# Performance work log

Measured on AMD Instinct MI355X. Metric: run time of the kernel, lower is better.

The kernel has to match this reference:

```python
import jax, jax.numpy as jnp
import numpy as np
import math

N_HEAD = 16
N_EMBD = 1024
N_LATENTS = 64
HEAD_DIM = N_EMBD // N_HEAD  # 64
ROPE_THETA = 10000.0


def setup_inputs() -> dict:
    key = jax.random.key(0)
    ks = jax.random.split(key, 6)
    B, T = 4, 4096
    x = jax.random.normal(ks[0], (B, T, N_EMBD), dtype=jnp.float32)
    # torch Linear weights applied as x @ W with W: [in, out] (equivalent up to init)
    s = 1.0 / math.sqrt(N_EMBD)
    Wk = jax.random.normal(ks[1], (N_EMBD, N_EMBD), dtype=jnp.float32) * s
    Wv = jax.random.normal(ks[2], (N_EMBD, N_EMBD), dtype=jnp.float32) * s
    Wg = jax.random.normal(ks[3], (N_EMBD, N_HEAD * N_LATENTS), dtype=jnp.float32) * s
    Wp = jax.random.normal(ks[4], (N_EMBD, N_EMBD), dtype=jnp.float32) * s
    latent_q = jax.random.normal(ks[5], (1, N_LATENTS, N_HEAD, HEAD_DIM), dtype=jnp.float32)
    return {"x": x, "latent_q": latent_q, "Wk": Wk, "Wv": Wv, "Wg": Wg, "Wp": Wp}


def _rope_interleaved(k, theta):
    # k: [B, T, H, D]; interleaved pairs rotated by position-dependent angles
    B, T, H, D = k.shape
    inv_freq = 1.0 / (theta ** (jnp.arange(0, D, 2, dtype=jnp.float32) / D))  # [D/2]
    ang = jnp.arange(T, dtype=jnp.float32)[:, None] * inv_freq[None, :]       # [T, D/2]
    cos = jnp.cos(ang)[None, :, None, :]
    sin = jnp.sin(ang)[None, :, None, :]
    k2 = k.reshape(B, T, H, D // 2, 2)
    kr = jnp.stack([k2[..., 0] * cos - k2[..., 1] * sin,
                    k2[..., 0] * sin + k2[..., 1] * cos], axis=-1)
    return kr.reshape(B, T, H, D).astype(k.dtype)


def reference(x, latent_q, Wk, Wv, Wg, Wp):
    B, T, C = x.shape
    H, D, L = N_HEAD, HEAD_DIM, N_LATENTS
    k = (x @ Wk).reshape(B, T, H, D)
    v = (x @ Wv).reshape(B, T, H, D)
    gates = jax.nn.softmax((x @ Wg).reshape(B, T, H, L), axis=-1)  # [B,T,H,L]
    k = _rope_interleaved(k, ROPE_THETA)
    q = jnp.broadcast_to(latent_q, (B, L, H, D)).transpose(0, 2, 1, 3)  # [B,H,L,D]
    kt = k.transpose(0, 2, 1, 3)  # [B,H,T,D]
    vt = v.transpose(0, 2, 1, 3)  # [B,H,T,D]
    scale = 1.0 / jnp.sqrt(jnp.asarray(D, dtype=x.dtype))
    scores = jnp.einsum('bhld,bhtd->bhlt', q, kt) * scale  # [B,H,L,T]
    # PyTorch SDPA is_causal with L_q != L_kv: top-left aligned tril(ones(L, T))
    causal = jnp.arange(T)[None, :] <= jnp.arange(L)[:, None]  # [L,T]
    scores = jnp.where(causal[None, None], scores, -jnp.inf)
    attn = jax.nn.softmax(scores, axis=-1)
    attn_out = jnp.einsum('bhlt,bhtd->bhld', attn, vt)  # [B,H,L,D]
    gates_t = gates.transpose(0, 2, 1, 3)  # [B,H,T,L]
    weighted = jnp.einsum('bhld,bhtl->bhtd', attn_out, gates_t)  # [B,H,T,D]
    out = weighted.transpose(0, 2, 1, 3).reshape(B, T, C)
    return out @ Wp
```

## Files before the change

### kernel.cpp

```cpp
#include <hip/hip_runtime.h>
#include <hip/hip_bf16.h>


typedef __attribute__((ext_vector_type(8))) short bf16x8;
typedef __attribute__((ext_vector_type(4))) float f32x4;
typedef __attribute__((ext_vector_type(4))) unsigned short us4;

__device__ __forceinline__ void gll16(const void* g, void* l) {
  __builtin_amdgcn_global_load_lds((const __attribute__((address_space(1))) void*)g,
                                   (__attribute__((address_space(3))) void*)l, 16, 0, 0);
}

__global__ __launch_bounds__(256)
void prep_kernel(const float* __restrict__ x, __hip_bfloat16* __restrict__ xb,
                 const float* __restrict__ Wg, const float* __restrict__ Wk,
                 const float* __restrict__ Wv, const float* __restrict__ Wp,
                 __hip_bfloat16* __restrict__ WgT, __hip_bfloat16* __restrict__ WkT,
                 __hip_bfloat16* __restrict__ WvT, __hip_bfloat16* __restrict__ WpT) {
  const int bid = blockIdx.x, tid = threadIdx.x;
  if (bid < 2048) {
    const int stride = 2048 * 256;
    for (int i = bid * 256 + tid; i < 4194304; i += stride) {
      float4 f = reinterpret_cast<const float4*>(x)[i];
      union { __hip_bfloat16 h[4]; us4 v; } u;
      u.h[0] = __float2bfloat16(f.x);
      u.h[1] = __float2bfloat16(f.y);
      u.h[2] = __float2bfloat16(f.z);
      u.h[3] = __float2bfloat16(f.w);
      reinterpret_cast<us4*>(xb)[i] = u.v;
    }
  } else {
    const int t = bid - 2048;
    const int z = t >> 10, rem = t & 1023;
    const float* W = (z == 0) ? Wg : ((z == 1) ? Wk : ((z == 2) ? Wv : Wp));
    __hip_bfloat16* Wt = (z == 0) ? WgT : ((z == 1) ? WkT : ((z == 2) ? WvT : WpT));
    __shared__ float tile[32][33];
    const int bx = (rem & 31) * 32, by = (rem >> 5) * 32;
    const int tx = tid & 31, ty = tid >> 5;
    #pragma unroll
    for (int j = 0; j < 32; j += 8)
      tile[ty + j][tx] = W[(size_t)(by + ty + j) * 1024 + bx + tx];
    __syncthreads();
    #pragma unroll
    for (int j = 0; j < 32; j += 8)
      Wt[(size_t)(bx + ty + j) * 1024 + by + tx] = __float2bfloat16(tile[tx][ty + j]);
  }
}

__global__ __launch_bounds__(256, 4)
void gemm128d(const __hip_bfloat16* __restrict__ A, const __hip_bfloat16* __restrict__ Bt,
              __hip_bfloat16* __restrict__ G) {
  __shared__ __align__(16) unsigned short SA[2][128 * 32];
  __shared__ __align__(16) unsigned short SB[2][128 * 32];
  const int tid = threadIdx.x;
  const int lane = tid & 63;
  const int w = tid >> 6;
  const int wm = w >> 1, wn = w & 1;
  const int lr = lane & 15, lk = lane >> 4;
  const int m0 = blockIdx.x * 128, n0 = blockIdx.y * 128;
  const int K = 1024;

  f32x4 acc[4][4] = {};

  auto STAGE = [&](int bsel, int kt) {
    #pragma unroll
    for (int r = 0; r < 2; ++r) {
      int c = r * 256 + tid;
      int row = c >> 2, slot = c & 3;
      int gs = slot ^ ((row >> 1) & 3);
      gll16(A + (size_t)(m0 + row) * K + kt + gs * 8, (char*)&SA[bsel][0] + c * 16);
      gll16(Bt + (size_t)(n0 + row) * K + kt + gs * 8, (char*)&SB[bsel][0] + c * 16);
    }
  };

  STAGE(0, 0);
  __syncthreads();

  int buf = 0;
  for (int t = 0; t < 32; ++t) {
    if (t + 1 < 32) STAGE(buf ^ 1, (t + 1) << 5);

    bf16x8 bfr[4];
    #pragma unroll
    for (int ni = 0; ni < 4; ++ni) {
      int row = wn * 64 + ni * 16 + lr;
      int ch = lk ^ ((row >> 1) & 3);
      bfr[ni] = *(const bf16x8*)&SB[buf][row * 32 + ch * 8];
    }
    #pragma unroll
    for (int mi = 0; mi < 4; ++mi) {
      int row = wm * 64 + mi * 16 + lr;
      int ch = lk ^ ((row >> 1) & 3);
      bf16x8 a = *(const bf16x8*)&SA[buf][row * 32 + ch * 8];
      #pragma unroll
      for (int ni = 0; ni < 4; ++ni)
        acc[mi][ni] = __builtin_amdgcn_mfma_f32_16x16x32_bf16(a, bfr[ni], acc[mi][ni], 0, 0, 0);
    }
    __syncthreads();
    buf ^= 1;
  }

  #pragma unroll
  for (int mi = 0; mi < 4; ++mi) {
    #pragma unroll
    for (int jj = 0; jj < 4; ++jj) {
      float mx = -3.0e38f;
      #pragma unroll
      for (int ni = 0; ni < 4; ++ni) mx = fmaxf(mx, acc[mi][ni][jj]);
      mx = fmaxf(mx, __shfl_xor(mx, 1));
      mx = fmaxf(mx, __shfl_xor(mx, 2));
      mx = fmaxf(mx, __shfl_xor(mx, 4));
      mx = fmaxf(mx, __shfl_xor(mx, 8));
      float e[4];
      float s = 0.f;
      #pragma unroll
      for (int ni = 0; ni < 4; ++ni) { e[ni] = __expf(acc[mi][ni][jj] - mx); s += e[ni]; }
      s += __shfl_xor(s, 1);
      s += __shfl_xor(s, 2);
      s += __shfl_xor(s, 4);
      s += __shfl_xor(s, 8);
      float inv = 1.0f / s;
      int r = m0 + wm * 64 + mi * 16 + lk * 4 + jj;
      #pragma unroll
      for (int ni = 0; ni < 4; ++ni)
        G[(size_t)r * 1024 + n0 + wn * 64 + ni * 16 + lr] = __float2bfloat16(e[ni] * inv);
    }
  }
}

__global__ __launch_bounds__(512, 2)
void gemm256o(const __hip_bfloat16* __restrict__ A, const __hip_bfloat16* __restrict__ Bt,
              float* __restrict__ Cv, int K, int ldc,
              long long astride, long long bstride, long long cstride) {
  __shared__ __align__(16) unsigned short SA[2][256 * 64];
  __shared__ __align__(16) unsigned short SB[2][256 * 64];
  const int tid = threadIdx.x;
  const int lane = tid & 63;
  const int w = tid >> 6;
  const int wm = w >> 2, wn = w & 3;
  const int lr = lane & 15, lk = lane >> 4;
  const int m0 = blockIdx.x * 256, n0 = blockIdx.y * 256;
  const long long b = blockIdx.z;
  const __hip_bfloat16* Ab = A + b * astride;
  const __hip_bfloat16* Bb = Bt + b * bstride;

  f32x4 acc[8][4] = {};

  const int NT = K >> 6;
  int buf = 0;

  auto STAGE = [&](int bsel, int kt) {
    #pragma unroll
    for (int r = 0; r < 4; ++r) {
      int c = r * 512 + tid;
      int row = c >> 3, slot = c & 7;
      int gch = slot ^ (row & 7);
      gll16(Ab + (size_t)(m0 + row) * K + kt + gch * 8, (char*)&SA[bsel][0] + c * 16);
      gll16(Bb + (size_t)(n0 + row) * K + kt + gch * 8, (char*)&SB[bsel][0] + c * 16);
    }
  };

  STAGE(0, 0);
  __syncthreads();

  for (int t = 0; t < NT; ++t) {
    if (t + 1 < NT) STAGE(buf ^ 1, (t + 1) << 6);

    bf16x8 bfr[2][4];
    #pragma unroll
    for (int kk = 0; kk < 2; ++kk)
      #pragma unroll
      for (int ni = 0; ni < 4; ++ni) {
        int row = wn * 64 + ni * 16 + lr;
        int ch = (kk * 4 + lk) ^ (row & 7);
        bfr[kk][ni] = *(const bf16x8*)&SB[buf][row * 64 + ch * 8];
      }
    #pragma unroll
    for (int mi = 0; mi < 8; ++mi) {
      int row = wm * 128 + mi * 16 + lr;
      int ch0 = lk ^ (row & 7);
      int ch1 = (4 + lk) ^ (row & 7);
      bf16x8 a0 = *(const bf16x8*)&SA[buf][row * 64 + ch0 * 8];
      bf16x8 a1 = *(const bf16x8*)&SA[buf][row * 64 + ch1 * 8];
      #pragma unroll
      for (int ni = 0; ni < 4; ++ni)
        acc[mi][ni] = __builtin_amdgcn_mfma_f32_16x16x32_bf16(a0, bfr[0][ni], acc[mi][ni], 0, 0, 0);
      #pragma unroll
      for (int ni = 0; ni < 4; ++ni)
        acc[mi][ni] = __builtin_amdgcn_mfma_f32_16x16x32_bf16(a1, bfr[1][ni], acc[mi][ni], 0, 0, 0);
    }
    __syncthreads();
    buf ^= 1;
  }

  float* C = Cv + b * cstride;
  #pragma unroll
  for (int mi = 0; mi < 8; ++mi) {
    int r = m0 + wm * 128 + mi * 16 + lk * 4;
    #pragma unroll
    for (int ni = 0; ni < 4; ++ni) {
      int c = n0 + wn * 64 + ni * 16 + lr;
      #pragma unroll
      for (int jj = 0; jj < 4; ++jj)
        C[(size_t)(r + jj) * ldc + c] = acc[mi][ni][jj];
    }
  }
}

__global__ __launch_bounds__(256)
void gemm_kv(const __hip_bfloat16* __restrict__ A, const __hip_bfloat16* __restrict__ Bt,
             float* __restrict__ kvp) {
  __shared__ __align__(16) unsigned short As[128 * 32];
  __shared__ __align__(16) unsigned short Bs[128 * 32];
  const int tid = threadIdx.x;
  const int lane = tid & 63;
  const int w = tid >> 6;
  const int wm = w >> 1, wn = w & 1;
  const int lr = lane & 15, lk = lane >> 4;
  const int m0 = blockIdx.x * 128, n0 = blockIdx.y * 128;
  const int ks = blockIdx.z;
  const int K = 1024;

  f32x4 acc[4][4] = {};
  const int r0 = tid >> 2;
  const int c8 = (tid & 3) * 8;

  auto xrow = [&](int rg) { return (size_t)(rg >> 6) * 4096 + (rg & 63); };

  for (int ki = 0; ki < 4; ++ki) {
    int kt = ks * 128 + ki * 32;
    __syncthreads();
    gll16(A + xrow(m0 + r0) * K + kt + c8,      (char*)As + (w * 64) * 16);
    gll16(Bt + (size_t)(n0 + r0) * K + kt + c8, (char*)Bs + (w * 64) * 16);
    gll16(A + xrow(m0 + 64 + r0) * K + kt + c8,      (char*)As + (256 + w * 64) * 16);
    gll16(Bt + (size_t)(n0 + 64 + r0) * K + kt + c8, (char*)Bs + (256 + w * 64) * 16);
    __syncthreads();

    bf16x8 af[4], bf[4];
    #pragma unroll
    for (int mi = 0; mi < 4; ++mi)
      af[mi] = *(const bf16x8*)&As[(wm * 64 + mi * 16 + lr) * 32 + lk * 8];
    #pragma unroll
    for (int ni = 0; ni < 4; ++ni)
      bf[ni] = *(const bf16x8*)&Bs[(wn * 64 + ni * 16 + lr) * 32 + lk * 8];
    #pragma unroll
    for (int mi = 0; mi < 4; ++mi)
      #pragma unroll
      for (int ni = 0; ni < 4; ++ni)
        acc[mi][ni] = __builtin_amdgcn_mfma_f32_16x16x32_bf16(af[mi], bf[ni], acc[mi][ni], 0, 0, 0);
  }

  float* C = kvp + (size_t)ks * 256 * 2048;
  #pragma unroll
  for (int mi = 0; mi < 4; ++mi) {
    int r = m0 + wm * 64 + mi * 16 + lk * 4;
    #pragma unroll
    for (int ni = 0; ni < 4; ++ni) {
      int c = n0 + wn * 64 + ni * 16 + lr;
      #pragma unroll
      for (int jj = 0; jj < 4; ++jj)
        C[(size_t)(r + jj) * 2048 + c] = acc[mi][ni][jj];
    }
  }
}

__global__ __launch_bounds__(256)
void attn_mt(const float* __restrict__ kvp, const float* __restrict__ lq,
             const __hip_bfloat16* __restrict__ WpT, __hip_bfloat16* __restrict__ Mt) {
  const int ct = blockIdx.x, h = blockIdx.y, b = blockIdx.z;
  __shared__ float Ks[64][64];
  __shared__ float Vs[64][64];
  __shared__ float S[64][65];
  __shared__ float Pt[64][65];
  __shared__ __align__(16) unsigned short SW[256 * 64];
  __shared__ __align__(16) unsigned short SAo[64 * 64];
  const int tid = threadIdx.x;
  const int lane = tid & 63;
  const int w = tid >> 6;
  const int lr = lane & 15, lk = lane >> 4;

  #pragma unroll
  for (int j = 0; j < 8; ++j) {
    int c2 = j * 256 + tid;
    int row = c2 >> 3, slot = c2 & 7;
    int gch = slot ^ (row & 7);
    gll16(WpT + (size_t)(ct * 256 + row) * 1024 + h * 64 + gch * 8, (char*)SW + c2 * 16);
  }

  {
    int r = tid >> 4;
    int c4 = (tid & 15) * 4;
    int i0 = c4 >> 1;
    float inv0 = exp2f(-13.287712379549449f * ((float)i0 * (1.0f / 32.0f)));
    float inv1 = exp2f(-13.287712379549449f * ((float)(i0 + 1) * (1.0f / 32.0f)));
    #pragma unroll
    for (int j = 0; j < 4; ++j) {
      int row = j * 16 + r;
      float4 kf = make_float4(0.f, 0.f, 0.f, 0.f);
      float4 vf = make_float4(0.f, 0.f, 0.f, 0.f);
      #pragma unroll
      for (int ks = 0; ks < 8; ++ks) {
        const float* base = kvp + ((size_t)ks * 256 + b * 64 + row) * 2048 + h * 64;
        float4 kp = *(const float4*)(base + c4);
        float4 vp = *(const float4*)(base + 1024 + c4);
        kf.x += kp.x; kf.y += kp.y; kf.z += kp.z; kf.w += kp.w;
        vf.x += vp.x; vf.y += vp.y; vf.z += vp.z; vf.w += vp.w;
      }
      float a0 = (float)row * inv0, a1 = (float)row * inv1;
      float s0 = sinf(a0), c0 = cosf(a0), s1 = sinf(a1), c1 = cosf(a1);
      *(float4*)&Ks[row][c4] = make_float4(kf.x * c0 - kf.y * s0, kf.x * s0 + kf.y * c0,
                                           kf.z * c1 - kf.w * s1, kf.z * s1 + kf.w * c1);
      *(float4*)&Vs[row][c4] = vf;
    }
  }
  __syncthreads();

  {
    const int l = tid & 63;
    float q[64];
    const float4* lq4 = (const float4*)(lq + ((size_t)l * 16 + h) * 64);
    #pragma unroll
    for (int i = 0; i < 16; ++i) {
      float4 f = lq4[i];
      q[4 * i] = f.x; q[4 * i + 1] = f.y; q[4 * i + 2] = f.z; q[4 * i + 3] = f.w;
    }
    #pragma unroll
    for (int tl = 0; tl < 16; ++tl) {
      int t = w * 16 + tl;
      float a = 0.f;
      #pragma unroll
      for (int d4 = 0; d4 < 16; ++d4) {
        float4 kf = *(const float4*)&Ks[t][d4 * 4];
        a += q[4 * d4] * kf.x + q[4 * d4 + 1] * kf.y + q[4 * d4 + 2] * kf.z + q[4 * d4 + 3] * kf.w;
      }
      S[l][t] = a * 0.125f;
    }
  }
  __syncthreads();

  {
    const int l = tid >> 2, c = tid & 3;
    float sv[16];
    float mx = -3.0e38f;
    #pragma unroll
    for (int i = 0; i < 16; ++i) {
      int t = c * 16 + i;
      sv[i] = S[l][t];
      if (t <= l) mx = fmaxf(mx, sv[i]);
    }
    mx = fmaxf(mx, __shfl_xor(mx, 1));
    mx = fmaxf(mx, __shfl_xor(mx, 2));
    float sum = 0.f;
    float e[16];
    #pragma unroll
    for (int i = 0; i < 16; ++i) {
      int t = c * 16 + i;
      e[i] = (t <= l) ? __expf(sv[i] - mx) : 0.f;
      sum += e[i];
    }
    sum += __shfl_xor(sum, 1);
    sum += __shfl_xor(sum, 2);
    float inv = 1.0f / sum;
    #pragma unroll
    for (int i = 0; i < 16; ++i) Pt[c * 16 + i][l] = e[i] * inv;
  }
  __syncthreads();

  {
    const int l = tid & 63;
    float o[16];
    #pragma unroll
    for (int i = 0; i < 16; ++i) o[i] = 0.f;
    for (int t = 0; t < 64; ++t) {
      float p = Pt[t][l];
      #pragma unroll
      for (int d4 = 0; d4 < 4; ++d4) {
        float4 vf = *(const float4*)&Vs[t][w * 16 + d4 * 4];
        o[4 * d4]     += p * vf.x;
        o[4 * d4 + 1] += p * vf.y;
        o[4 * d4 + 2] += p * vf.z;
        o[4 * d4 + 3] += p * vf.w;
      }
    }
    union { __hip_bfloat16 hh[8]; bf16x8 v; } p0, p1;
    #pragma unroll
    for (int i = 0; i < 8; ++i) { p0.hh[i] = __float2bfloat16(o[i]); p1.hh[i] = __float2bfloat16(o[8 + i]); }
    *(bf16x8*)&SAo[l * 64 + ((2 * w) ^ (l & 7)) * 8]     = p0.v;
    *(bf16x8*)&SAo[l * 64 + ((2 * w + 1) ^ (l & 7)) * 8] = p1.v;
  }
  __syncthreads();

  f32x4 acc[4][4] = {};
  bf16x8 bfr[2][4];
  #pragma unroll
  for (int kk = 0; kk < 2; ++kk)
    #pragma unroll
    for (int ni = 0; ni < 4; ++ni) {
      int row = ni * 16 + lr;
      int ch = (kk * 4 + lk) ^ (row & 7);
      bfr[kk][ni] = *(const bf16x8*)&SAo[row * 64 + ch * 8];
    }
  #pragma unroll
  for (int mi = 0; mi < 4; ++mi) {
    int row = w * 64 + mi * 16 + lr;
    int ch0 = lk ^ (row & 7);
    int ch1 = (4 + lk) ^ (row & 7);
    bf16x8 a0 = *(const bf16x8*)&SW[row * 64 + ch0 * 8];
    bf16x8 a1 = *(const bf16x8*)&SW[row * 64 + ch1 * 8];
    #pragma unroll
    for (int ni = 0; ni < 4; ++ni)
      acc[mi][ni] = __builtin_amdgcn_mfma_f32_16x16x32_bf16(a0, bfr[0][ni], acc[mi][ni], 0, 0, 0);
    #pragma unroll
    for (int ni = 0; ni < 4; ++ni)
      acc[mi][ni] = __builtin_amdgcn_mfma_f32_16x16x32_bf16(a1, bfr[1][ni], acc[mi][ni], 0, 0, 0);
  }

  #pragma unroll
  for (int mi = 0; mi < 4; ++mi) {
    int c = ct * 256 + w * 64 + mi * 16 + lk * 4;
    #pragma unroll
    for (int ni = 0; ni < 4; ++ni) {
      int l = ni * 16 + lr;
      #pragma unroll
      for (int jj = 0; jj < 4; ++jj)
        Mt[((size_t)b * 1024 + c + jj) * 1024 + h * 64 + l] = __float2bfloat16(acc[mi][ni][jj]);
    }
  }
}

extern "C" void kernel_launch(void* const* d_in, const int* in_sizes, int n_in,
                              void* d_out, int out_size, void* d_ws, size_t ws_size,
                              hipStream_t stream) {
  const float* x  = (const float*)d_in[0];
  const float* lq = (const float*)d_in[1];
  const float* Wk = (const float*)d_in[2];
  const float* Wv = (const float*)d_in[3];
  const float* Wg = (const float*)d_in[4];
  const float* Wp = (const float*)d_in[5];
  float* out = (float*)d_out;

  char* w = (char*)d_ws;
  __hip_bfloat16* xb   = (__hip_bfloat16*)(w);
  __hip_bfloat16* G    = (__hip_bfloat16*)(w + 33554432);
  __hip_bfloat16* WgT  = (__hip_bfloat16*)(w + 67108864);
  __hip_bfloat16* WkvT = (__hip_bfloat16*)(w + 69206016);
  __hip_bfloat16* WpT  = (__hip_bfloat16*)(w + 73400320);
  __hip_bfloat16* Mt   = (__hip_bfloat16*)(w + 75497472);
  float* kvp = out;

  prep_kernel<<<6144, 256, 0, stream>>>(x, xb, Wg, Wk, Wv, Wp,
                                        WgT, WkvT, WkvT + 1024 * 1024, WpT);

  gemm128d<<<dim3(128, 8), 256, 0, stream>>>(xb, WgT, G);

  gemm_kv<<<dim3(2, 16, 8), 256, 0, stream>>>(xb, WkvT, kvp);

  attn_mt<<<dim3(4, 16, 4), 256, 0, stream>>>(kvp, lq, WpT, Mt);

  gemm256o<<<dim3(16, 4, 4), 512, 0, stream>>>(G, Mt, out, 1024, 1024,
                                               4096LL * 1024, 1024LL * 1024, 4096LL * 1024);
}
```

Baseline: 135.1 us.

## Retile gate GEMM to 256x256 tiles with 32x32x16 MFMA and fused softmax

The gate projection GEMM with its fused per-head softmax now uses 256x256 output tiles, a K step of 64 and 512-thread blocks instead of 128x128 tiles and 256 threads. It switches from 16x16x32 to 32x32x16 bf16 MFMA and uses a new XOR swizzle on the LDS layout. The softmax epilogue is rewritten for the 32-wide MFMA output layout, so each 64-latent head row is now reduced across 32 lanes. The goal is more data reuse per LDS load and fewer global loads. In exchange, the block needs 128 KB of LDS, so only one block fits per CU, the grid drops to 256 blocks, and there is less latency hiding.

Result: slower. 140.9 us (+4.3%).

```diff
diff --git a/kernel.cpp b/kernel.cpp
--- a/kernel.cpp
+++ b/kernel.cpp
@@ -4,6 +4,7 @@
 
 typedef __attribute__((ext_vector_type(8))) short bf16x8;
 typedef __attribute__((ext_vector_type(4))) float f32x4;
+typedef __attribute__((ext_vector_type(16))) float f32x16;
 typedef __attribute__((ext_vector_type(4))) unsigned short us4;
 
 __device__ __forceinline__ void gll16(const void* g, void* l) {
@@ -47,29 +48,29 @@
   }
 }
 
-__global__ __launch_bounds__(256, 4)
-void gemm128d(const __hip_bfloat16* __restrict__ A, const __hip_bfloat16* __restrict__ Bt,
+__global__ __launch_bounds__(512, 2)
+void gemm_g32(const __hip_bfloat16* __restrict__ A, const __hip_bfloat16* __restrict__ Bt,
               __hip_bfloat16* __restrict__ G) {
-  __shared__ __align__(16) unsigned short SA[2][128 * 32];
-  __shared__ __align__(16) unsigned short SB[2][128 * 32];
+  __shared__ __align__(16) unsigned short SA[2][256 * 64];
+  __shared__ __align__(16) unsigned short SB[2][256 * 64];
   const int tid = threadIdx.x;
   const int lane = tid & 63;
   const int w = tid >> 6;
-  const int wm = w >> 1, wn = w & 1;
-  const int lr = lane & 15, lk = lane >> 4;
-  const int m0 = blockIdx.x * 128, n0 = blockIdx.y * 128;
+  const int wm = w >> 2, wn = w & 3;
+  const int l5 = lane & 31, hi = lane >> 5;
+  const int m0 = blockIdx.x * 256, n0 = blockIdx.y * 256;
   const int K = 1024;
 
-  f32x4 acc[4][4] = {};
+  f32x16 acc[4][2] = {};
 
   auto STAGE = [&](int bsel, int kt) {
     #pragma unroll
-    for (int r = 0; r < 2; ++r) {
-      int c = r * 256 + tid;
-      int row = c >> 2, slot = c & 3;
-      int gs = slot ^ ((row >> 1) & 3);
-      gll16(A + (size_t)(m0 + row) * K + kt + gs * 8, (char*)&SA[bsel][0] + c * 16);
-      gll16(Bt + (size_t)(n0 + row) * K + kt + gs * 8, (char*)&SB[bsel][0] + c * 16);
+    for (int r = 0; r < 4; ++r) {
+      int c = r * 512 + tid;
+      int row = c >> 3, slot = c & 7;
+      int gch = slot ^ (row & 7);
+      gll16(A + (size_t)(m0 + row) * K + kt + gch * 8, (char*)&SA[bsel][0] + c * 16);
+      gll16(Bt + (size_t)(n0 + row) * K + kt + gch * 8, (char*)&SB[bsel][0] + c * 16);
     }
   };
 
@@ -77,24 +78,29 @@
   __syncthreads();
 
   int buf = 0;
-  for (int t = 0; t < 32; ++t) {
-    if (t + 1 < 32) STAGE(buf ^ 1, (t + 1) << 5);
-
-    bf16x8 bfr[4];
-    #pragma unroll
-    for (int ni = 0; ni < 4; ++ni) {
-      int row = wn * 64 + ni * 16 + lr;
-      int ch = lk ^ ((row >> 1) & 3);
-      bfr[ni] = *(const bf16x8*)&SB[buf][row * 32 + ch * 8];
-    }
-    #pragma unroll
-    for (int mi = 0; mi < 4; ++mi) {
-      int row = wm * 64 + mi * 16 + lr;
-      int ch = lk ^ ((row >> 1) & 3);
-      bf16x8 a = *(const bf16x8*)&SA[buf][row * 32 + ch * 8];
-      #pragma unroll
-      for (int ni = 0; ni < 4; ++ni)
-        acc[mi][ni] = __builtin_amdgcn_mfma_f32_16x16x32_bf16(a, bfr[ni], acc[mi][ni], 0, 0, 0);
+  for (int t = 0; t < 16; ++t) {
+    if (t + 1 < 16) STAGE(buf ^ 1, (t + 1) << 6);
+
+    #pragma unroll
+    for (int kk = 0; kk < 4; ++kk) {
+      const int kc = kk * 2 + hi;
+      bf16x8 b0, b1, a[4];
+      {
+        int row = wn * 64 + l5;
+        b0 = *(const bf16x8*)&SB[buf][row * 64 + (kc ^ (row & 7)) * 8];
+        row = wn * 64 + 32 + l5;
+        b1 = *(const bf16x8*)&SB[buf][row * 64 + (kc ^ (row & 7)) * 8];
+      }
+      #pragma unroll
+      for (int mi = 0; mi < 4; ++mi) {
+        int row = wm * 128 + mi * 32 + l5;
+        a[mi] = *(const bf16x8*)&SA[buf][row * 64 + (kc ^ (row & 7)) * 8];
+      }
+      #pragma unroll
+      for (int mi = 0; mi < 4; ++mi) {
+        acc[mi][0] = __builtin_amdgcn_mfma_f32_32x32x16_bf16(a[mi], b0, acc[mi][0], 0, 0, 0);
+        acc[mi][1] = __builtin_amdgcn_mfma_f32_32x32x16_bf16(a[mi], b1, acc[mi][1], 0, 0, 0);
+      }
     }
     __syncthreads();
     buf ^= 1;
@@ -103,27 +109,25 @@
   #pragma unroll
   for (int mi = 0; mi < 4; ++mi) {
     #pragma unroll
-    for (int jj = 0; jj < 4; ++jj) {
-      float mx = -3.0e38f;
-      #pragma unroll
-      for (int ni = 0; ni < 4; ++ni) mx = fmaxf(mx, acc[mi][ni][jj]);
+    for (int r = 0; r < 16; ++r) {
+      float v0 = acc[mi][0][r], v1 = acc[mi][1][r];
+      float mx = fmaxf(v0, v1);
       mx = fmaxf(mx, __shfl_xor(mx, 1));
       mx = fmaxf(mx, __shfl_xor(mx, 2));
       mx = fmaxf(mx, __shfl_xor(mx, 4));
       mx = fmaxf(mx, __shfl_xor(mx, 8));
-      float e[4];
-      float s = 0.f;
-      #pragma unroll
-      for (int ni = 0; ni < 4; ++ni) { e[ni] = __expf(acc[mi][ni][jj] - mx); s += e[ni]; }
+      mx = fmaxf(mx, __shfl_xor(mx, 16));
+      float e0 = __expf(v0 - mx), e1 = __expf(v1 - mx);
+      float s = e0 + e1;
       s += __shfl_xor(s, 1);
       s += __shfl_xor(s, 2);
       s += __shfl_xor(s, 4);
       s += __shfl_xor(s, 8);
+      s += __shfl_xor(s, 16);
       float inv = 1.0f / s;
-      int r = m0 + wm * 64 + mi * 16 + lk * 4 + jj;
-      #pragma unroll
-      for (int ni = 0; ni < 4; ++ni)
-        G[(size_t)r * 1024 + n0 + wn * 64 + ni * 16 + lr] = __float2bfloat16(e[ni] * inv);
+      int row = m0 + wm * 128 + mi * 32 + (r & 3) + 8 * (r >> 2) + 4 * hi;
+      G[(size_t)row * 1024 + n0 + wn * 64 + l5]      = __float2bfloat16(e0 * inv);
+      G[(size_t)row * 1024 + n0 + wn * 64 + 32 + l5] = __float2bfloat16(e1 * inv);
     }
   }
 }
@@ -451,7 +455,7 @@
   prep_kernel<<<6144, 256, 0, stream>>>(x, xb, Wg, Wk, Wv, Wp,
                                         WgT, WkvT, WkvT + 1024 * 1024, WpT);
 
-  gemm128d<<<dim3(128, 8), 256, 0, stream>>>(xb, WgT, G);
+  gemm_g32<<<dim3(64, 4), 512, 0, stream>>>(xb, WgT, G);
 
   gemm_kv<<<dim3(2, 16, 8), 256, 0, stream>>>(xb, WkvT, kvp);
 
```
